# Optimization experiments

Measured on AMD Instinct MI355X. Metric: run time of the kernel, lower is better.

Reference implementation:

```python
import jax, jax.numpy as jnp
import numpy as np

B, S, D_IN, D_OUT, DEPTH = 4, 2048, 2048, 2048, 11
N_NODES = 2 ** (DEPTH + 1) - 1  # 4095


def setup_inputs() -> dict:
    key = jax.random.key(0)
    k1, k2, k3 = jax.random.split(key, 3)
    x = jax.random.normal(k1, (B, S, D_IN), dtype=jnp.float32)
    # scale weights like Linear init (~1/sqrt(fan_in)) to keep logits sane
    w_in = jax.random.normal(k2, (N_NODES, D_IN), dtype=jnp.float32) * (1.0 / np.sqrt(D_IN))
    w_out = jax.random.normal(k3, (D_OUT, N_NODES), dtype=jnp.float32) * (1.0 / np.sqrt(N_NODES))
    return {"x": x, "w_in": w_in, "w_out": w_out}


def reference(x, w_in, w_out):
    # x: [B,S,D_in]; w_in: [n_nodes, D_in]; w_out: [D_out, n_nodes]
    b, s, _ = x.shape
    cur = jnp.zeros((b, s), dtype=jnp.int32)
    nodes, logits = [], []
    for _ in range(DEPTH + 1):  # fixed, small depth loop (12 iters)
        nodes.append(cur)
        coeffs = w_in[cur]                       # [B,S,D_in] data-dependent gather
        score = jnp.einsum('bsd,bsd->bs', x, coeffs)  # per-token dot product
        logits.append(score)
        cur = cur * 2 + (score >= 0).astype(jnp.int32) + 1
    all_nodes = jnp.stack(nodes, axis=-1)        # [B,S,depth+1]
    all_logits = jnp.stack(logits, axis=-1)      # [B,S,depth+1]
    sel = w_out.T[all_nodes]                     # [B,S,depth+1,D_out]
    mlp1 = jax.nn.gelu(all_logits, approximate=False)  # torch nn.GELU default = exact erf
    return jnp.einsum('bsl,bslw->bsw', mlp1, sel)      # [B,S,D_out]
```

## Files before the change

### kernel.cpp

```cpp
#include <hip/hip_runtime.h>


#define D_IN    2048
#define D_OUT   2048
#define DEPTHP1 12
#define N_NODES 4095
#define N_TOK   8192
#define N_LEAF  2048

__global__ __launch_bounds__(256) void fusedA2(
    const float* __restrict__ x,
    const float* __restrict__ w_in,
    const float* __restrict__ w_out,
    float* __restrict__ w_out_t,
    float* __restrict__ s_all,
    int* __restrict__ leaf,
    int* __restrict__ hist) {
    if (blockIdx.x & 1) {
        __shared__ float tile[64][65];
        const int tb = blockIdx.x >> 1;
        const int n0 = (tb & 63) * 64;
        const int j0 = (tb >> 6) * 64;
        const int tx = threadIdx.x & 63;
        const int ty = threadIdx.x >> 6;
        const int n = n0 + tx;
#pragma unroll
        for (int k = 0; k < 16; k++) {
            const int r = ty * 16 + k;
            if (n < N_NODES) tile[r][tx] = w_out[(size_t)(j0 + r) * N_NODES + n];
        }
        __syncthreads();
#pragma unroll
        for (int k = 0; k < 16; k++) {
            const int r = ty * 16 + k;
            const int nn = n0 + r;
            if (nn < N_NODES) w_out_t[(size_t)nn * D_OUT + (j0 + tx)] = tile[tx][r];
        }
        return;
    }

    const int wave  = threadIdx.x >> 6;
    const int lane  = threadIdx.x & 63;
    const int token = (blockIdx.x >> 1) * 4 + wave;

    const float4* xrow = (const float4*)(x + (size_t)token * D_IN);
    float4 xf[8];
#pragma unroll
    for (int c = 0; c < 8; c++) xf[c] = xrow[lane + 64 * c];

    int cur = 0;
#pragma unroll
    for (int l = 0; l < DEPTHP1; l++) {
        const float4* wrow = (const float4*)(w_in + (size_t)cur * D_IN);
        float4 wv[8];
#pragma unroll
        for (int c = 0; c < 8; c++) wv[c] = wrow[lane + 64 * c];
        float p0 = 0.f, p1 = 0.f, p2 = 0.f, p3 = 0.f;
#pragma unroll
        for (int c = 0; c < 8; c++) {
            float* p = (c < 2) ? &p0 : (c < 4) ? &p1 : (c < 6) ? &p2 : &p3;
            *p += wv[c].x * xf[c].x + wv[c].y * xf[c].y +
                  wv[c].z * xf[c].z + wv[c].w * xf[c].w;
        }
        float part = (p0 + p1) + (p2 + p3);
#pragma unroll
        for (int off = 32; off >= 1; off >>= 1)
            part += __shfl_xor(part, off, 64);
        const float score = part;
        cur = 2 * cur + 1 + (score >= 0.f ? 1 : 0);
        if (lane == 0) s_all[token * DEPTHP1 + l] = score;
    }
    if (lane == 0) {
        const int leafid = ((cur - 1) >> 1) - (N_LEAF - 1);
        leaf[token] = leafid;
        atomicAdd(&hist[leafid], 1);
    }
}

__global__ __launch_bounds__(256) void init_counts(int* __restrict__ p) {
    const int i = blockIdx.x * 256 + threadIdx.x;
    if (i < 2 * N_LEAF) p[i] = 0;
}

__global__ __launch_bounds__(256) void scan2048(
    const int* __restrict__ hist, int* __restrict__ offsets ) {
    __shared__ int vals[N_LEAF];
    __shared__ int partial[256];
    const int t = threadIdx.x;
    int sum = 0;
#pragma unroll
    for (int k = 0; k < 8; k++) {
        const int v = hist[t * 8 + k];
        vals[t * 8 + k] = v;
        sum += v;
    }
    partial[t] = sum;
    __syncthreads();
    for (int off = 1; off < 256; off <<= 1) {
        const int v  = partial[t];
        const int vo = (t >= off) ? partial[t - off] : 0;
        __syncthreads();
        partial[t] = v + vo;
        __syncthreads();
    }
    int base = (t > 0) ? partial[t - 1] : 0;
#pragma unroll
    for (int k = 0; k < 8; k++) {
        offsets[t * 8 + k] = base;
        base += vals[t * 8 + k];
    }
    if (t == 255) offsets[N_LEAF] = base;
}

__global__ __launch_bounds__(256) void scatter_tokens2(
    const int* __restrict__ leaf, const int* __restrict__ offsets,
    int* __restrict__ cnt, const float* __restrict__ s_all,
    int* __restrict__ order, float* __restrict__ g_sorted) {
    const int t = blockIdx.x * 256 + threadIdx.x;
    if (t < N_TOK) {
        const int lf = leaf[t];
        const int pos = offsets[lf] + atomicAdd(&cnt[lf], 1);
        order[pos] = t;
#pragma unroll
        for (int l = 0; l < DEPTHP1; l++) {
            const float s = s_all[(size_t)t * DEPTHP1 + l];
            const float g = 0.5f * s * (1.0f + erff(s * 0.70710678118654752f));
            g_sorted[(size_t)pos * DEPTHP1 + l] = g;
        }
    }
}

__global__ __launch_bounds__(256, 2) void phaseB3(
    const float* __restrict__ w_out_t,
    const float* __restrict__ g_sorted,
    const int* __restrict__ order,
    const int* __restrict__ offsets,
    float* __restrict__ out) {
    const int lf = ((blockIdx.x & 7) << 8) | (blockIdx.x >> 3);
    const int start = offsets[lf];
    const int end   = offsets[lf + 1];
    if (start == end) return;
    const int t = threadIdx.x;

    __shared__ float gs[96];
    __shared__ int   ord[8];

    int nodes[DEPTHP1];
    const int L = lf + N_LEAF;
#pragma unroll
    for (int l = 0; l < DEPTHP1; l++) nodes[l] = (L >> (DEPTHP1 - 1 - l)) - 1;

    float4 w0[DEPTHP1], w1[DEPTHP1];
#pragma unroll
    for (int l = 0; l < DEPTHP1; l++) {
        const float4* wr = (const float4*)(w_out_t + (size_t)nodes[l] * D_OUT);
        w0[l] = wr[t * 2 + 0];
        w1[l] = wr[t * 2 + 1];
    }

    for (int cs = start; cs < end; cs += 8) {
        const int T = end - cs;
        __syncthreads();
        if (t < 96 && (size_t)cs * 12 + t < (size_t)end * 12)
            gs[t] = g_sorted[(size_t)cs * 12 + t];
        if (t >= 96 && t < 104 && cs + (t - 96) < end)
            ord[t - 96] = order[cs + (t - 96)];
        __syncthreads();

        float acc[8][8];
#pragma unroll
        for (int tt = 0; tt < 8; tt++)
#pragma unroll
            for (int k = 0; k < 8; k++) acc[tt][k] = 0.f;

#pragma unroll
        for (int l = 0; l < DEPTHP1; l++) {
#pragma unroll
            for (int tt = 0; tt < 8; tt++) {
                const float g = (tt < T) ? gs[tt * DEPTHP1 + l] : 0.f;
                acc[tt][0] += g * w0[l].x; acc[tt][1] += g * w0[l].y;
                acc[tt][2] += g * w0[l].z; acc[tt][3] += g * w0[l].w;
                acc[tt][4] += g * w1[l].x; acc[tt][5] += g * w1[l].y;
                acc[tt][6] += g * w1[l].z; acc[tt][7] += g * w1[l].w;
            }
        }
#pragma unroll
        for (int tt = 0; tt < 8; tt++) {
            if (tt < T) {
                const int tok = ord[tt];
                float4* po = (float4*)(out + (size_t)tok * D_OUT + t * 8);
                float4 o0, o1;
                o0.x = acc[tt][0]; o0.y = acc[tt][1];
                o0.z = acc[tt][2]; o0.w = acc[tt][3];
                o1.x = acc[tt][4]; o1.y = acc[tt][5];
                o1.z = acc[tt][6]; o1.w = acc[tt][7];
                po[0] = o0; po[1] = o1;
            }
        }
    }
}

__global__ __launch_bounds__(256) void transpose_wout64(
    const float* __restrict__ in, float* __restrict__ out) {
    __shared__ float tile[64][65];
    const int n0 = blockIdx.x * 64;
    const int j0 = blockIdx.y * 64;
    const int tx = threadIdx.x;
    const int ty = threadIdx.y;
    const int n = n0 + tx;
#pragma unroll
    for (int k = 0; k < 16; k++) {
        const int r = ty * 16 + k;
        if (n < N_NODES) tile[r][tx] = in[(size_t)(j0 + r) * N_NODES + n];
    }
    __syncthreads();
#pragma unroll
    for (int k = 0; k < 16; k++) {
        const int r = ty * 16 + k;
        const int nn = n0 + r;
        if (nn < N_NODES) out[(size_t)nn * D_OUT + (j0 + tx)] = tile[tx][r];
    }
}

template <bool TRANSPOSED>
__global__ __launch_bounds__(256) void fff_fused(
    const float* __restrict__ x, const float* __restrict__ w_in,
    const float* __restrict__ w_out, float* __restrict__ out) {
    const int wave  = threadIdx.x >> 6;
    const int lane  = threadIdx.x & 63;
    const int token = blockIdx.x * 4 + wave;
    const float4* xrow = (const float4*)(x + (size_t)token * D_IN);
    float xf[32];
#pragma unroll
    for (int c = 0; c < 8; c++) {
        float4 xc = xrow[lane + 64 * c];
        xf[c * 4 + 0] = xc.x; xf[c * 4 + 1] = xc.y;
        xf[c * 4 + 2] = xc.z; xf[c * 4 + 3] = xc.w;
    }
    float acc[32];
#pragma unroll
    for (int k = 0; k < 32; k++) acc[k] = 0.f;
    int cur = 0;
#pragma unroll
    for (int l = 0; l < DEPTHP1; l++) {
        const float4* wrow = (const float4*)(w_in + (size_t)cur * D_IN);
        float part = 0.f;
#pragma unroll
        for (int c = 0; c < 8; c++) {
            float4 wc = wrow[lane + 64 * c];
            part += wc.x * xf[c * 4 + 0]; part += wc.y * xf[c * 4 + 1];
            part += wc.z * xf[c * 4 + 2]; part += wc.w * xf[c * 4 + 3];
        }
#pragma unroll
        for (int off = 32; off >= 1; off >>= 1) part += __shfl_xor(part, off, 64);
        const float score = part;
        const float g = 0.5f * score * (1.0f + erff(score * 0.70710678118654752f));
        if (TRANSPOSED) {
            const float4* orow = (const float4*)(w_out + (size_t)cur * D_OUT);
#pragma unroll
            for (int c = 0; c < 8; c++) {
                float4 oc = orow[lane + 64 * c];
                acc[c * 4 + 0] += g * oc.x; acc[c * 4 + 1] += g * oc.y;
                acc[c * 4 + 2] += g * oc.z; acc[c * 4 + 3] += g * oc.w;
            }
        } else {
#pragma unroll
            for (int c = 0; c < 8; c++)
#pragma unroll
                for (int k = 0; k < 4; k++) {
                    const int j = (lane + 64 * c) * 4 + k;
                    acc[c * 4 + k] += g * w_out[(size_t)j * N_NODES + cur];
                }
        }
        cur = 2 * cur + 1 + (score >= 0.f ? 1 : 0);
    }
    float4* outrow = (float4*)(out + (size_t)token * D_OUT);
#pragma unroll
    for (int c = 0; c < 8; c++) {
        float4 o;
        o.x = acc[c * 4 + 0]; o.y = acc[c * 4 + 1];
        o.z = acc[c * 4 + 2]; o.w = acc[c * 4 + 3];
        outrow[lane + 64 * c] = o;
    }
}

extern "C" void kernel_launch(void* const* d_in, const int* in_sizes, int n_in,
                              void* d_out, int out_size, void* d_ws, size_t ws_size,
                              hipStream_t stream) {
    (void)in_sizes; (void)n_in; (void)out_size;
    const float* x     = (const float*)d_in[0];
    const float* w_in  = (const float*)d_in[1];
    const float* w_out = (const float*)d_in[2];
    float* out = (float*)d_out;

    const size_t wt_bytes   = (size_t)N_NODES * D_OUT * sizeof(float);
    const size_t g_bytes    = (size_t)N_TOK * DEPTHP1 * sizeof(float);
    const size_t leaf_bytes = (size_t)N_TOK * sizeof(int);
    const size_t ord_bytes  = (size_t)N_TOK * sizeof(int);
    const size_t hist_bytes = (size_t)N_LEAF * sizeof(int);
    const size_t cnt_bytes  = (size_t)N_LEAF * sizeof(int);
    const size_t offs_bytes = (size_t)(N_LEAF + 1) * sizeof(int);
    const size_t gs_bytes   = g_bytes;
    const size_t need = wt_bytes + g_bytes + leaf_bytes + ord_bytes +
                        hist_bytes + cnt_bytes + offs_bytes + gs_bytes + 64;

    if (ws_size >= need) {
        char* p = (char*)d_ws;
        float* w_out_t  = (float*)p;  p += wt_bytes;
        float* s_all    = (float*)p;  p += g_bytes;
        int*   leaf     = (int*)p;    p += leaf_bytes;
        int*   order    = (int*)p;    p += ord_bytes;
        int*   hist     = (int*)p;    p += hist_bytes;
        int*   cnt      = (int*)p;    p += cnt_bytes;
        int*   offsets  = (int*)p;    p += offs_bytes;
        float* g_sorted = (float*)p;

        init_counts<<<(2 * N_LEAF + 255) / 256, 256, 0, stream>>>(hist);
        fusedA2<<<4096, 256, 0, stream>>>(x, w_in, w_out, w_out_t,
                                          s_all, leaf, hist);
        scan2048<<<1, 256, 0, stream>>>(hist, offsets);
        scatter_tokens2<<<N_TOK / 256, 256, 0, stream>>>(leaf, offsets, cnt,
                                                         s_all, order, g_sorted);
        phaseB3<<<N_LEAF, 256, 0, stream>>>(w_out_t, g_sorted, order, offsets, out);
    } else if (ws_size >= wt_bytes) {
        float* w_out_t = (float*)d_ws;
        transpose_wout64<<<dim3((N_NODES + 63) / 64, D_OUT / 64), dim3(64, 4),
                           0, stream>>>(w_out, w_out_t);
        fff_fused<true><<<N_TOK / 4, 256, 0, stream>>>(x, w_in, w_out_t, out);
    } else {
        fff_fused<false><<<N_TOK / 4, 256, 0, stream>>>(x, w_in, w_out, out);
    }
}
```

Before: 261.2 us.

## Group four sibling leaves per block in phase B with LDS-staged weights

The output phase now gives each block four adjacent leaves. Their shared ancestor rows plus the distinct level-10 and level-11 nodes (16 rows) are staged into 64KB of LDS in two halves. Each token's gelu coefficients are scattered into 16 slots, so one blocked loop serves all four leaves and the w_out_t ancestor reads are amortised. The routing kernel switches to inline-asm global loads with a scalar base via readfirstlane, and writes the scores as vectors. The large LDS footprint lowers occupancy, and the grid drops from 2048 to 512 blocks.

```diff
diff --git a/kernel.cpp b/kernel.cpp
--- a/kernel.cpp
+++ b/kernel.cpp
@@ -8,7 +8,9 @@
 #define N_TOK   8192
 #define N_LEAF  2048
 
-__global__ __launch_bounds__(256) void fusedA2(
+typedef float f4 __attribute__((ext_vector_type(4)));
+
+__global__ __launch_bounds__(256, 4) void fusedA3(
     const float* __restrict__ x,
     const float* __restrict__ w_in,
     const float* __restrict__ w_out,
@@ -48,29 +50,52 @@
 #pragma unroll
     for (int c = 0; c < 8; c++) xf[c] = xrow[lane + 64 * c];
 
+    const unsigned voffA = (unsigned)lane * 16u;
+    const unsigned voffB = voffA + 4096u;
+
     int cur = 0;
+    float sc[DEPTHP1];
 #pragma unroll
     for (int l = 0; l < DEPTHP1; l++) {
-        const float4* wrow = (const float4*)(w_in + (size_t)cur * D_IN);
-        float4 wv[8];
-#pragma unroll
-        for (int c = 0; c < 8; c++) wv[c] = wrow[lane + 64 * c];
+        const float* wbase = w_in + (size_t)cur * D_IN;
+        f4 w0, w1, w2, w3, w4, w5, w6, w7;
+        asm volatile("global_load_dwordx4 %0, %1, %2"             : "=v"(w0) : "v"(voffA), "s"(wbase));
+        asm volatile("global_load_dwordx4 %0, %1, %2 offset:1024" : "=v"(w1) : "v"(voffA), "s"(wbase));
+        asm volatile("global_load_dwordx4 %0, %1, %2 offset:2048" : "=v"(w2) : "v"(voffA), "s"(wbase));
+        asm volatile("global_load_dwordx4 %0, %1, %2 offset:3072" : "=v"(w3) : "v"(voffA), "s"(wbase));
+        asm volatile("global_load_dwordx4 %0, %1, %2"             : "=v"(w4) : "v"(voffB), "s"(wbase));
+        asm volatile("global_load_dwordx4 %0, %1, %2 offset:1024" : "=v"(w5) : "v"(voffB), "s"(wbase));
+        asm volatile("global_load_dwordx4 %0, %1, %2 offset:2048" : "=v"(w6) : "v"(voffB), "s"(wbase));
+        asm volatile("global_load_dwordx4 %0, %1, %2 offset:3072" : "=v"(w7) : "v"(voffB), "s"(wbase));
+        asm volatile("s_waitcnt vmcnt(0)"
+                     : "+v"(w0), "+v"(w1), "+v"(w2), "+v"(w3),
+                       "+v"(w4), "+v"(w5), "+v"(w6), "+v"(w7)
+                     :: "memory");
+
         float p0 = 0.f, p1 = 0.f, p2 = 0.f, p3 = 0.f;
-#pragma unroll
-        for (int c = 0; c < 8; c++) {
-            float* p = (c < 2) ? &p0 : (c < 4) ? &p1 : (c < 6) ? &p2 : &p3;
-            *p += wv[c].x * xf[c].x + wv[c].y * xf[c].y +
-                  wv[c].z * xf[c].z + wv[c].w * xf[c].w;
-        }
+        p0 += w0[0]*xf[0].x + w0[1]*xf[0].y + w0[2]*xf[0].z + w0[3]*xf[0].w;
+        p0 += w1[0]*xf[1].x + w1[1]*xf[1].y + w1[2]*xf[1].z + w1[3]*xf[1].w;
+        p1 += w2[0]*xf[2].x + w2[1]*xf[2].y + w2[2]*xf[2].z + w2[3]*xf[2].w;
+        p1 += w3[0]*xf[3].x + w3[1]*xf[3].y + w3[2]*xf[3].z + w3[3]*xf[3].w;
+        p2 += w4[0]*xf[4].x + w4[1]*xf[4].y + w4[2]*xf[4].z + w4[3]*xf[4].w;
+        p2 += w5[0]*xf[5].x + w5[1]*xf[5].y + w5[2]*xf[5].z + w5[3]*xf[5].w;
+        p3 += w6[0]*xf[6].x + w6[1]*xf[6].y + w6[2]*xf[6].z + w6[3]*xf[6].w;
+        p3 += w7[0]*xf[7].x + w7[1]*xf[7].y + w7[2]*xf[7].z + w7[3]*xf[7].w;
         float part = (p0 + p1) + (p2 + p3);
 #pragma unroll
         for (int off = 32; off >= 1; off >>= 1)
             part += __shfl_xor(part, off, 64);
         const float score = part;
-        cur = 2 * cur + 1 + (score >= 0.f ? 1 : 0);
-        if (lane == 0) s_all[token * DEPTHP1 + l] = score;
+        cur = __builtin_amdgcn_readfirstlane(
+                  2 * cur + 1 + (score >= 0.f ? 1 : 0));
+        sc[l] = score;
     }
     if (lane == 0) {
+        f4* sp = (f4*)(s_all + (size_t)token * DEPTHP1);
+        f4 a = {sc[0], sc[1], sc[2],  sc[3]};
+        f4 b = {sc[4], sc[5], sc[6],  sc[7]};
+        f4 c = {sc[8], sc[9], sc[10], sc[11]};
+        sp[0] = a; sp[1] = b; sp[2] = c;
         const int leafid = ((cur - 1) >> 1) - (N_LEAF - 1);
         leaf[token] = leafid;
         atomicAdd(&hist[leafid], 1);
@@ -112,15 +137,17 @@
     if (t == 255) offsets[N_LEAF] = base;
 }
 
-__global__ __launch_bounds__(256) void scatter_tokens2(
+__global__ __launch_bounds__(256) void scatter_tokens3(
     const int* __restrict__ leaf, const int* __restrict__ offsets,
     int* __restrict__ cnt, const float* __restrict__ s_all,
-    int* __restrict__ order, float* __restrict__ g_sorted) {
+    int* __restrict__ order, float* __restrict__ g_sorted,
+    int* __restrict__ lf_sorted) {
     const int t = blockIdx.x * 256 + threadIdx.x;
     if (t < N_TOK) {
         const int lf = leaf[t];
         const int pos = offsets[lf] + atomicAdd(&cnt[lf], 1);
         order[pos] = t;
+        lf_sorted[pos] = lf;
 #pragma unroll
         for (int l = 0; l < DEPTHP1; l++) {
             const float s = s_all[(size_t)t * DEPTHP1 + l];
@@ -130,71 +157,81 @@
     }
 }
 
-__global__ __launch_bounds__(256, 2) void phaseB3(
+__global__ __launch_bounds__(256, 2) void phaseB4(
     const float* __restrict__ w_out_t,
     const float* __restrict__ g_sorted,
+    const int* __restrict__ lf_sorted,
     const int* __restrict__ order,
     const int* __restrict__ offsets,
     float* __restrict__ out) {
-    const int lf = ((blockIdx.x & 7) << 8) | (blockIdx.x >> 3);
-    const int start = offsets[lf];
-    const int end   = offsets[lf + 1];
+    const int grp = ((blockIdx.x & 7) << 6) | (blockIdx.x >> 3);
+    const int lf0 = grp * 4;
+    const int start = offsets[lf0];
+    const int end   = offsets[lf0 + 4];
     if (start == end) return;
     const int t = threadIdx.x;
 
-    __shared__ float gs[96];
-    __shared__ int   ord[8];
-
-    int nodes[DEPTHP1];
-    const int L = lf + N_LEAF;
-#pragma unroll
-    for (int l = 0; l < DEPTHP1; l++) nodes[l] = (L >> (DEPTHP1 - 1 - l)) - 1;
-
-    float4 w0[DEPTHP1], w1[DEPTHP1];
-#pragma unroll
-    for (int l = 0; l < DEPTHP1; l++) {
-        const float4* wr = (const float4*)(w_out_t + (size_t)nodes[l] * D_OUT);
-        w0[l] = wr[t * 2 + 0];
-        w1[l] = wr[t * 2 + 1];
-    }
-
-    for (int cs = start; cs < end; cs += 8) {
-        const int T = end - cs;
-        __syncthreads();
-        if (t < 96 && (size_t)cs * 12 + t < (size_t)end * 12)
-            gs[t] = g_sorted[(size_t)cs * 12 + t];
-        if (t >= 96 && t < 104 && cs + (t - 96) < end)
-            ord[t - 96] = order[cs + (t - 96)];
-        __syncthreads();
-
-        float acc[8][8];
-#pragma unroll
-        for (int tt = 0; tt < 8; tt++)
-#pragma unroll
-            for (int k = 0; k < 8; k++) acc[tt][k] = 0.f;
-
-#pragma unroll
-        for (int l = 0; l < DEPTHP1; l++) {
+    __shared__ float wlds[16 * 1024];
+    __shared__ float gslot[2][8][16];
+    __shared__ int   ordl[2][8];
+
+    int node[16];
+    const int base1 = lf0 + N_LEAF;
+#pragma unroll
+    for (int l = 0; l <= 9; l++) node[l] = (base1 >> (11 - l)) - 1;
+    node[10] = (base1 >> 1) - 1;
+    node[11] = (base1 >> 1);
+    node[12] = base1 - 1;
+    node[13] = base1;
+    node[14] = base1 + 1;
+    node[15] = base1 + 2;
+
+    for (int half = 0; half < 2; half++) {
+        __syncthreads();
+#pragma unroll
+        for (int k = 0; k < 16; k++)
+            ((f4*)wlds)[k * 256 + t] =
+                ((const f4*)(w_out_t + (size_t)node[k] * D_OUT + half * 1024))[t];
+        __syncthreads();
+
+        int buf = 0;
+        for (int cs = start; cs < end; cs += 8, buf ^= 1) {
+            if (t < 8) {
+                const int pos = cs + t;
+#pragma unroll
+                for (int s = 0; s < 16; s++) gslot[buf][t][s] = 0.f;
+                if (pos < end) {
+                    const int lf = lf_sorted[pos];
+#pragma unroll
+                    for (int l = 0; l <= 9; l++)
+                        gslot[buf][t][l] = g_sorted[(size_t)pos * DEPTHP1 + l];
+                    gslot[buf][t][10 + ((lf >> 1) & 1)] =
+                        g_sorted[(size_t)pos * DEPTHP1 + 10];
+                    gslot[buf][t][12 + (lf & 3)] =
+                        g_sorted[(size_t)pos * DEPTHP1 + 11];
+                    ordl[buf][t] = order[pos];
+                }
+            }
+            __syncthreads();
+            const int T = end - cs;
+            f4 acc[8];
+#pragma unroll
+            for (int tt = 0; tt < 8; tt++) acc[tt] = (f4)0.f;
+#pragma unroll
+            for (int r = 0; r < 16; r++) {
+                const f4 w = ((const f4*)wlds)[r * 256 + t];
+#pragma unroll
+                for (int tt = 0; tt < 8; tt++) {
+                    const float g = gslot[buf][tt][r];
+                    acc[tt] += g * w;
+                }
+            }
 #pragma unroll
             for (int tt = 0; tt < 8; tt++) {
-                const float g = (tt < T) ? gs[tt * DEPTHP1 + l] : 0.f;
-                acc[tt][0] += g * w0[l].x; acc[tt][1] += g * w0[l].y;
-                acc[tt][2] += g * w0[l].z; acc[tt][3] += g * w0[l].w;
-                acc[tt][4] += g * w1[l].x; acc[tt][5] += g * w1[l].y;
-                acc[tt][6] += g * w1[l].z; acc[tt][7] += g * w1[l].w;
-            }
-        }
-#pragma unroll
-        for (int tt = 0; tt < 8; tt++) {
-            if (tt < T) {
-                const int tok = ord[tt];
-                float4* po = (float4*)(out + (size_t)tok * D_OUT + t * 8);
-                float4 o0, o1;
-                o0.x = acc[tt][0]; o0.y = acc[tt][1];
-                o0.z = acc[tt][2]; o0.w = acc[tt][3];
-                o1.x = acc[tt][4]; o1.y = acc[tt][5];
-                o1.z = acc[tt][6]; o1.w = acc[tt][7];
-                po[0] = o0; po[1] = o1;
+                if (tt < T) {
+                    const int tok = ordl[buf][tt];
+                    ((f4*)(out + (size_t)tok * D_OUT + half * 1024))[t] = acc[tt];
+                }
             }
         }
     }
@@ -301,8 +338,10 @@
     const size_t cnt_bytes  = (size_t)N_LEAF * sizeof(int);
     const size_t offs_bytes = (size_t)(N_LEAF + 1) * sizeof(int);
     const size_t gs_bytes   = g_bytes;
+    const size_t lfs_bytes  = (size_t)N_TOK * sizeof(int);
     const size_t need = wt_bytes + g_bytes + leaf_bytes + ord_bytes +
-                        hist_bytes + cnt_bytes + offs_bytes + gs_bytes + 64;
+                        hist_bytes + cnt_bytes + offs_bytes + gs_bytes +
+                        lfs_bytes + 64;
 
     if (ws_size >= need) {
         char* p = (char*)d_ws;
@@ -313,15 +352,18 @@
         int*   hist     = (int*)p;    p += hist_bytes;
         int*   cnt      = (int*)p;    p += cnt_bytes;
         int*   offsets  = (int*)p;    p += offs_bytes;
-        float* g_sorted = (float*)p;
+        float* g_sorted = (float*)p;  p += gs_bytes;
+        int*   lf_sorted= (int*)p;
 
         init_counts<<<(2 * N_LEAF + 255) / 256, 256, 0, stream>>>(hist);
-        fusedA2<<<4096, 256, 0, stream>>>(x, w_in, w_out, w_out_t,
+        fusedA3<<<4096, 256, 0, stream>>>(x, w_in, w_out, w_out_t,
                                           s_all, leaf, hist);
         scan2048<<<1, 256, 0, stream>>>(hist, offsets);
-        scatter_tokens2<<<N_TOK / 256, 256, 0, stream>>>(leaf, offsets, cnt,
-                                                         s_all, order, g_sorted);
-        phaseB3<<<N_LEAF, 256, 0, stream>>>(w_out_t, g_sorted, order, offsets, out);
+        scatter_tokens3<<<N_TOK / 256, 256, 0, stream>>>(leaf, offsets, cnt,
+                                                         s_all, order, g_sorted,
+                                                         lf_sorted);
+        phaseB4<<<512, 256, 0, stream>>>(w_out_t, g_sorted, lf_sorted, order,
+                                         offsets, out);
     } else if (ws_size >= wt_bytes) {
         float* w_out_t = (float*)d_ws;
         transpose_wout64<<<dim3((N_NODES + 63) / 64, D_OUT / 64), dim3(64, 4),
```

Measured after the change: 261.7 us. About the same (+0.2%).

## Split tree traversal into two phases, grouping tokens by depth-3 subtree

Applied to the files above, without the earlier changes.

Tree traversal now runs in two phases. The first walks levels 0-2 per token and buckets tokens into 8 subtree groups. The remaining levels then run with blocks assigned per group, so w_in rows of that subtree stay cache-hot. The w_out transpose moves into its own kernel, which also zeroes the counters and replaces init_counts. phaseB drops its shared-memory staging and register-held weights in favour of direct loads, and uses nontemporal stores. The cost is extra launches, a second read of x, and an extra scatter pass.

```diff
diff --git a/kernel.cpp b/kernel.cpp
--- a/kernel.cpp
+++ b/kernel.cpp
@@ -7,60 +7,66 @@
 #define N_NODES 4095
 #define N_TOK   8192
 #define N_LEAF  2048
-
-__global__ __launch_bounds__(256) void fusedA2(
+#define A1_GPB  512
+
+typedef float f4 __attribute__((ext_vector_type(4)));
+
+__global__ __launch_bounds__(256) void transpose_wout64z(
+    const float* __restrict__ in, float* __restrict__ out,
+    int* __restrict__ hc ) {
+    __shared__ float tile[64][65];
+    const int fb = blockIdx.y * 64 + blockIdx.x;
+    const int tx = threadIdx.x;
+    const int ty = threadIdx.y;
+    if (fb < 17) {
+        const int i = fb * 256 + ty * 64 + tx;
+        if (i < 2 * N_LEAF + 16) hc[i] = 0;
+    }
+    const int n0 = blockIdx.x * 64;
+    const int j0 = blockIdx.y * 64;
+    const int n = n0 + tx;
+#pragma unroll
+    for (int k = 0; k < 16; k++) {
+        const int r = ty * 16 + k;
+        if (n < N_NODES) tile[r][tx] = in[(size_t)(j0 + r) * N_NODES + n];
+    }
+    __syncthreads();
+#pragma unroll
+    for (int k = 0; k < 16; k++) {
+        const int r = ty * 16 + k;
+        const int nn = n0 + r;
+        if (nn < N_NODES) out[(size_t)nn * D_OUT + (j0 + tx)] = tile[tx][r];
+    }
+}
+
+__global__ __launch_bounds__(256) void phaseA0(
     const float* __restrict__ x,
     const float* __restrict__ w_in,
-    const float* __restrict__ w_out,
-    float* __restrict__ w_out_t,
     float* __restrict__ s_all,
-    int* __restrict__ leaf,
-    int* __restrict__ hist) {
-    if (blockIdx.x & 1) {
-        __shared__ float tile[64][65];
-        const int tb = blockIdx.x >> 1;
-        const int n0 = (tb & 63) * 64;
-        const int j0 = (tb >> 6) * 64;
-        const int tx = threadIdx.x & 63;
-        const int ty = threadIdx.x >> 6;
-        const int n = n0 + tx;
-#pragma unroll
-        for (int k = 0; k < 16; k++) {
-            const int r = ty * 16 + k;
-            if (n < N_NODES) tile[r][tx] = w_out[(size_t)(j0 + r) * N_NODES + n];
-        }
-        __syncthreads();
-#pragma unroll
-        for (int k = 0; k < 16; k++) {
-            const int r = ty * 16 + k;
-            const int nn = n0 + r;
-            if (nn < N_NODES) w_out_t[(size_t)nn * D_OUT + (j0 + tx)] = tile[tx][r];
-        }
-        return;
-    }
-
+    int* __restrict__ grp8,
+    int* __restrict__ hist8) {
     const int wave  = threadIdx.x >> 6;
     const int lane  = threadIdx.x & 63;
-    const int token = (blockIdx.x >> 1) * 4 + wave;
-
-    const float4* xrow = (const float4*)(x + (size_t)token * D_IN);
-    float4 xf[8];
+    const int token = blockIdx.x * 4 + wave;
+
+    const f4* xrow = (const f4*)(x + (size_t)token * D_IN);
+    f4 xf[8];
 #pragma unroll
     for (int c = 0; c < 8; c++) xf[c] = xrow[lane + 64 * c];
 
     int cur = 0;
 #pragma unroll
-    for (int l = 0; l < DEPTHP1; l++) {
-        const float4* wrow = (const float4*)(w_in + (size_t)cur * D_IN);
-        float4 wv[8];
+    for (int l = 0; l < 3; l++) {
+        const f4* wrow = (const f4*)(w_in + (size_t)cur * D_IN);
+        f4 wv[8];
 #pragma unroll
         for (int c = 0; c < 8; c++) wv[c] = wrow[lane + 64 * c];
         float p0 = 0.f, p1 = 0.f, p2 = 0.f, p3 = 0.f;
 #pragma unroll
         for (int c = 0; c < 8; c++) {
             float* p = (c < 2) ? &p0 : (c < 4) ? &p1 : (c < 6) ? &p2 : &p3;
-            *p += wv[c].x * xf[c].x + wv[c].y * xf[c].y +
-                  wv[c].z * xf[c].z + wv[c].w * xf[c].w;
+            *p += wv[c][0] * xf[c][0] + wv[c][1] * xf[c][1] +
+                  wv[c][2] * xf[c][2] + wv[c][3] * xf[c][3];
         }
         float part = (p0 + p1) + (p2 + p3);
 #pragma unroll
@@ -71,15 +77,81 @@
         if (lane == 0) s_all[token * DEPTHP1 + l] = score;
     }
     if (lane == 0) {
-        const int leafid = ((cur - 1) >> 1) - (N_LEAF - 1);
-        leaf[token] = leafid;
-        atomicAdd(&hist[leafid], 1);
-    }
-}
-
-__global__ __launch_bounds__(256) void init_counts(int* __restrict__ p) {
-    const int i = blockIdx.x * 256 + threadIdx.x;
-    if (i < 2 * N_LEAF) p[i] = 0;
+        const int g = cur - 7;
+        grp8[token] = g;
+        atomicAdd(&hist8[g], 1);
+    }
+}
+
+__global__ __launch_bounds__(256) void scatter8(
+    const int* __restrict__ grp8, const int* __restrict__ hist8,
+    int* __restrict__ cnt8, int* __restrict__ order3,
+    int* __restrict__ offs8 ) {
+    const int t = blockIdx.x * 256 + threadIdx.x;
+    int base[8];
+    int acc = 0;
+#pragma unroll
+    for (int k = 0; k < 8; k++) { base[k] = acc; acc += hist8[k]; }
+    if (t < 8) offs8[t] = base[t];
+    if (t == 8) offs8[8] = N_TOK;
+    if (t < N_TOK) {
+        const int g = grp8[t];
+        const int pos = base[g] + atomicAdd(&cnt8[g], 1);
+        order3[pos] = t;
+    }
+}
+
+__global__ __launch_bounds__(256) void phaseA1(
+    const float* __restrict__ x,
+    const float* __restrict__ w_in,
+    const int* __restrict__ order3,
+    const int* __restrict__ offs8,
+    float* __restrict__ s_all,
+    int* __restrict__ leaf,
+    int* __restrict__ hist) {
+    const int g    = blockIdx.x & 7;
+    const int idx  = blockIdx.x >> 3;
+    const int wave = threadIdx.x >> 6;
+    const int lane = threadIdx.x & 63;
+    const int beg = offs8[g];
+    const int lim = offs8[g + 1];
+
+    for (int slot = beg + idx * 4 + wave; slot < lim; slot += 4 * A1_GPB) {
+        const int token = order3[slot];
+        const f4* xrow = (const f4*)(x + (size_t)token * D_IN);
+        f4 xf[8];
+#pragma unroll
+        for (int c = 0; c < 8; c++)
+            xf[c] = __builtin_nontemporal_load(&xrow[lane + 64 * c]);
+
+        int cur = g + 7;
+#pragma unroll
+        for (int l = 3; l < DEPTHP1; l++) {
+            const f4* wrow = (const f4*)(w_in + (size_t)cur * D_IN);
+            f4 wv[8];
+#pragma unroll
+            for (int c = 0; c < 8; c++) wv[c] = wrow[lane + 64 * c];
+            float p0 = 0.f, p1 = 0.f, p2 = 0.f, p3 = 0.f;
+#pragma unroll
+            for (int c = 0; c < 8; c++) {
+                float* p = (c < 2) ? &p0 : (c < 4) ? &p1 : (c < 6) ? &p2 : &p3;
+                *p += wv[c][0] * xf[c][0] + wv[c][1] * xf[c][1] +
+                      wv[c][2] * xf[c][2] + wv[c][3] * xf[c][3];
+            }
+            float part = (p0 + p1) + (p2 + p3);
+#pragma unroll
+            for (int off = 32; off >= 1; off >>= 1)
+                part += __shfl_xor(part, off, 64);
+            const float score = part;
+            cur = 2 * cur + 1 + (score >= 0.f ? 1 : 0);
+            if (lane == 0) s_all[token * DEPTHP1 + l] = score;
+        }
+        if (lane == 0) {
+            const int leafid = ((cur - 1) >> 1) - (N_LEAF - 1);
+            leaf[token] = leafid;
+            atomicAdd(&hist[leafid], 1);
+        }
+    }
 }
 
 __global__ __launch_bounds__(256) void scan2048(
@@ -130,7 +202,7 @@
     }
 }
 
-__global__ __launch_bounds__(256, 2) void phaseB3(
+__global__ __launch_bounds__(256, 2) void phaseB(
     const float* __restrict__ w_out_t,
     const float* __restrict__ g_sorted,
     const int* __restrict__ order,
@@ -142,31 +214,13 @@
     if (start == end) return;
     const int t = threadIdx.x;
 
-    __shared__ float gs[96];
-    __shared__ int   ord[8];
-
     int nodes[DEPTHP1];
     const int L = lf + N_LEAF;
 #pragma unroll
     for (int l = 0; l < DEPTHP1; l++) nodes[l] = (L >> (DEPTHP1 - 1 - l)) - 1;
 
-    float4 w0[DEPTHP1], w1[DEPTHP1];
-#pragma unroll
-    for (int l = 0; l < DEPTHP1; l++) {
-        const float4* wr = (const float4*)(w_out_t + (size_t)nodes[l] * D_OUT);
-        w0[l] = wr[t * 2 + 0];
-        w1[l] = wr[t * 2 + 1];
-    }
-
     for (int cs = start; cs < end; cs += 8) {
         const int T = end - cs;
-        __syncthreads();
-        if (t < 96 && (size_t)cs * 12 + t < (size_t)end * 12)
-            gs[t] = g_sorted[(size_t)cs * 12 + t];
-        if (t >= 96 && t < 104 && cs + (t - 96) < end)
-            ord[t - 96] = order[cs + (t - 96)];
-        __syncthreads();
-
         float acc[8][8];
 #pragma unroll
         for (int tt = 0; tt < 8; tt++)
@@ -175,26 +229,31 @@
 
 #pragma unroll
         for (int l = 0; l < DEPTHP1; l++) {
+            const float4* wr = (const float4*)(w_out_t + (size_t)nodes[l] * D_OUT);
+            const float4 w0 = wr[t * 2 + 0];
+            const float4 w1 = wr[t * 2 + 1];
 #pragma unroll
             for (int tt = 0; tt < 8; tt++) {
-                const float g = (tt < T) ? gs[tt * DEPTHP1 + l] : 0.f;
-                acc[tt][0] += g * w0[l].x; acc[tt][1] += g * w0[l].y;
-                acc[tt][2] += g * w0[l].z; acc[tt][3] += g * w0[l].w;
-                acc[tt][4] += g * w1[l].x; acc[tt][5] += g * w1[l].y;
-                acc[tt][6] += g * w1[l].z; acc[tt][7] += g * w1[l].w;
+                const float g = (tt < T)
+                    ? g_sorted[(size_t)(cs + tt) * DEPTHP1 + l] : 0.f;
+                acc[tt][0] += g * w0.x; acc[tt][1] += g * w0.y;
+                acc[tt][2] += g * w0.z; acc[tt][3] += g * w0.w;
+                acc[tt][4] += g * w1.x; acc[tt][5] += g * w1.y;
+                acc[tt][6] += g * w1.z; acc[tt][7] += g * w1.w;
             }
         }
 #pragma unroll
         for (int tt = 0; tt < 8; tt++) {
             if (tt < T) {
-                const int tok = ord[tt];
-                float4* po = (float4*)(out + (size_t)tok * D_OUT + t * 8);
-                float4 o0, o1;
-                o0.x = acc[tt][0]; o0.y = acc[tt][1];
-                o0.z = acc[tt][2]; o0.w = acc[tt][3];
-                o1.x = acc[tt][4]; o1.y = acc[tt][5];
-                o1.z = acc[tt][6]; o1.w = acc[tt][7];
-                po[0] = o0; po[1] = o1;
+                const int tok = order[cs + tt];
+                f4* po = (f4*)(out + (size_t)tok * D_OUT + t * 8);
+                f4 o0, o1;
+                o0[0] = acc[tt][0]; o0[1] = acc[tt][1];
+                o0[2] = acc[tt][2]; o0[3] = acc[tt][3];
+                o1[0] = acc[tt][4]; o1[1] = acc[tt][5];
+                o1[2] = acc[tt][6]; o1[3] = acc[tt][7];
+                __builtin_nontemporal_store(o0, po);
+                __builtin_nontemporal_store(o1, po + 1);
             }
         }
     }
@@ -294,34 +353,49 @@
     float* out = (float*)d_out;
 
     const size_t wt_bytes   = (size_t)N_NODES * D_OUT * sizeof(float);
-    const size_t g_bytes    = (size_t)N_TOK * DEPTHP1 * sizeof(float);
+    const size_t s_bytes    = (size_t)N_TOK * DEPTHP1 * sizeof(float);
     const size_t leaf_bytes = (size_t)N_TOK * sizeof(int);
     const size_t ord_bytes  = (size_t)N_TOK * sizeof(int);
-    const size_t hist_bytes = (size_t)N_LEAF * sizeof(int);
-    const size_t cnt_bytes  = (size_t)N_LEAF * sizeof(int);
+    const size_t hc_bytes   = (size_t)(2 * N_LEAF + 16) * sizeof(int);
+    const size_t off8_bytes = 16 * sizeof(int);
     const size_t offs_bytes = (size_t)(N_LEAF + 1) * sizeof(int);
-    const size_t gs_bytes   = g_bytes;
-    const size_t need = wt_bytes + g_bytes + leaf_bytes + ord_bytes +
-                        hist_bytes + cnt_bytes + offs_bytes + gs_bytes + 64;
+    const size_t gs_bytes   = s_bytes;
+    const size_t grp_bytes  = (size_t)N_TOK * sizeof(int);
+    const size_t o3_bytes   = (size_t)N_TOK * sizeof(int);
+    const size_t need = wt_bytes + s_bytes + leaf_bytes + ord_bytes +
+                        hc_bytes + off8_bytes + offs_bytes + gs_bytes +
+                        grp_bytes + o3_bytes + 64;
 
     if (ws_size >= need) {
         char* p = (char*)d_ws;
         float* w_out_t  = (float*)p;  p += wt_bytes;
-        float* s_all    = (float*)p;  p += g_bytes;
+        float* s_all    = (float*)p;  p += s_bytes;
+        float* g_sorted = (float*)p;  p += gs_bytes;
         int*   leaf     = (int*)p;    p += leaf_bytes;
         int*   order    = (int*)p;    p += ord_bytes;
-        int*   hist     = (int*)p;    p += hist_bytes;
-        int*   cnt      = (int*)p;    p += cnt_bytes;
+        int*   hist     = (int*)p;    p += 2 * N_LEAF * sizeof(int) - N_LEAF * sizeof(int);
+        p = (char*)hist;
+        int*   cnt      = hist + N_LEAF;
+        int*   hist8    = hist + 2 * N_LEAF;
+        int*   cnt8     = hist8 + 8;
+        p = (char*)(hist) + hc_bytes;
+        int*   offs8    = (int*)p;    p += off8_bytes;
         int*   offsets  = (int*)p;    p += offs_bytes;
-        float* g_sorted = (float*)p;
-
-        init_counts<<<(2 * N_LEAF + 255) / 256, 256, 0, stream>>>(hist);
-        fusedA2<<<4096, 256, 0, stream>>>(x, w_in, w_out, w_out_t,
-                                          s_all, leaf, hist);
+        int*   grp8     = (int*)p;    p += grp_bytes;
+        int*   order3   = (int*)p;
+
+        transpose_wout64z<<<dim3(64, 32), dim3(64, 4), 0, stream>>>(
+            w_out, w_out_t, hist);
+        phaseA0<<<N_TOK / 4, 256, 0, stream>>>(x, w_in, s_all, grp8, hist8);
+        scatter8<<<N_TOK / 256, 256, 0, stream>>>(grp8, hist8, cnt8, order3,
+                                                  offs8);
+        phaseA1<<<8 * A1_GPB, 256, 0, stream>>>(x, w_in, order3, offs8,
+                                                s_all, leaf, hist);
         scan2048<<<1, 256, 0, stream>>>(hist, offsets);
         scatter_tokens2<<<N_TOK / 256, 256, 0, stream>>>(leaf, offsets, cnt,
                                                          s_all, order, g_sorted);
-        phaseB3<<<N_LEAF, 256, 0, stream>>>(w_out_t, g_sorted, order, offsets, out);
+        phaseB<<<N_LEAF, 256, 0, stream>>>(w_out_t, g_sorted, order, offsets,
+                                           out);
     } else if (ws_size >= wt_bytes) {
         float* w_out_t = (float*)d_ws;
         transpose_wout64<<<dim3((N_NODES + 63) / 64, D_OUT / 64), dim3(64, 4),
```

Result: slower. 338.0 us (+29.4%).
